# Kernel optimization log

Measured on AMD Instinct MI355X. Metric: run time of the kernel, lower is better.

The kernel has to match this reference:

```python
import jax, jax.numpy as jnp
import numpy as np

H = 2048  # hidden_dim == input_dim


def _lstm_step(x, h, c, Wih, Whh, bih, bhh):
    # x: [1, in], h/c: [1, H]; PyTorch gate order: i, f, g, o along 4H axis
    gates = x @ Wih.T + h @ Whh.T + bih + bhh  # [1, 4H]
    i, f, g, o = jnp.split(gates, 4, axis=-1)
    c2 = jax.nn.sigmoid(f) * c + jax.nn.sigmoid(i) * jnp.tanh(g)
    h2 = jax.nn.sigmoid(o) * jnp.tanh(c2)
    return h2, c2


def setup_inputs() -> dict:
    key = jax.random.key(0)
    ks = jax.random.split(key, 20)
    s = 0.02
    inp = {
        "x": jax.random.normal(ks[0], (1,), dtype=jnp.float32),
        "input_hidden": jax.random.normal(ks[1], (3, 1, H), dtype=jnp.float32),
        "input_cell": jax.random.normal(ks[2], (3, 1, H), dtype=jnp.float32),
        # layer 0: input_size = 1
        "Wih0": jax.random.normal(ks[3], (4 * H, 1), dtype=jnp.float32) * s,
        "Whh0": jax.random.normal(ks[4], (4 * H, H), dtype=jnp.float32) * s,
        "bih0": jax.random.normal(ks[5], (4 * H,), dtype=jnp.float32) * s,
        "bhh0": jax.random.normal(ks[6], (4 * H,), dtype=jnp.float32) * s,
        # layers 1, 2: input_size = H
        "Wih1": jax.random.normal(ks[7], (4 * H, H), dtype=jnp.float32) * s,
        "Whh1": jax.random.normal(ks[8], (4 * H, H), dtype=jnp.float32) * s,
        "bih1": jax.random.normal(ks[9], (4 * H,), dtype=jnp.float32) * s,
        "bhh1": jax.random.normal(ks[10], (4 * H,), dtype=jnp.float32) * s,
        "Wih2": jax.random.normal(ks[11], (4 * H, H), dtype=jnp.float32) * s,
        "Whh2": jax.random.normal(ks[12], (4 * H, H), dtype=jnp.float32) * s,
        "bih2": jax.random.normal(ks[13], (4 * H,), dtype=jnp.float32) * s,
        "bhh2": jax.random.normal(ks[14], (4 * H,), dtype=jnp.float32) * s,
        # output projection: Linear(H, 1)
        "Wout": jax.random.normal(ks[15], (1, H), dtype=jnp.float32) * s,
        "bout": jax.random.normal(ks[16], (1,), dtype=jnp.float32) * s,
    }
    return inp


def reference(x, input_hidden, input_cell,
              Wih0, Whh0, bih0, bhh0,
              Wih1, Whh1, bih1, bhh1,
              Wih2, Whh2, bih2, bhh2,
              Wout, bout):
    # x.reshape((1,1,1)) in torch -> single timestep, batch 1, feature 1
    inp = x.reshape(1, 1)  # [batch=1, in=1]
    params = [(Wih0, Whh0, bih0, bhh0),
              (Wih1, Whh1, bih1, bhh1),
              (Wih2, Whh2, bih2, bhh2)]
    hs, cs = [], []
    layer_in = inp
    for l, (Wih, Whh, bih, bhh) in enumerate(params):  # fixed 3 layers
        h2, c2 = _lstm_step(layer_in, input_hidden[l], input_cell[l], Wih, Whh, bih, bhh)
        hs.append(h2)
        cs.append(c2)
        layer_in = h2
    hidden_n = jnp.stack(hs, axis=0)  # [3, 1, H]
    cell_n = jnp.stack(cs, axis=0)    # [3, 1, H]
    # top-layer output [1,1,H] -> Linear -> [1,1,1]
    y = (layer_in @ Wout.T + bout).reshape(1, 1, 1)
    return y, hidden_n, cell_n
```

## Files before the change

### kernel.cpp

```cpp
#include <hip/hip_runtime.h>
#include <math.h>

#define H 2048

__device__ __forceinline__ float sigmoidf_(float v) {
    return 1.0f / (1.0f + expf(-v));
}

__device__ __forceinline__ float dot4(float4 a, float4 b) {
    return a.x * b.x + a.y * b.y + a.z * b.z + a.w * b.w;
}

__device__ __forceinline__ void bfly4(float& a, float& b, float& c, float& d) {
#pragma unroll
    for (int off = 32; off > 0; off >>= 1) {
        a += __shfl_down(a, off, 64);
        b += __shfl_down(b, off, 64);
        c += __shfl_down(c, off, 64);
        d += __shfl_down(d, off, 64);
    }
}

__global__ __launch_bounds__(256, 4)
void lstm_layer(const float* __restrict__ Wih, const float* __restrict__ Whh,
                const float* __restrict__ bih, const float* __restrict__ bhh,
                const float* __restrict__ xin,
                const float* __restrict__ hin,
                const float* __restrict__ cin,
                float* __restrict__ hout, float* __restrict__ cout)
{
    const int t    = blockIdx.x;
    const int tid  = threadIdx.x;
    const int w    = tid >> 6;
    const int lane = tid & 63;
    const int idx  = (w << 7) + lane;

    const float b_i = bih[t]         + bhh[t];
    const float b_f = bih[H + t]     + bhh[H + t];
    const float b_g = bih[2 * H + t] + bhh[2 * H + t];
    const float b_o = bih[3 * H + t] + bhh[3 * H + t];
    const float cprev = cin[t];

    const float4* x4  = (const float4*)xin;
    const float4* h4  = (const float4*)hin;
    const float4* wi0 = (const float4*)(Wih + (size_t)t * H);
    const float4* wh0 = (const float4*)(Whh + (size_t)t * H);
    const float4* wi1 = (const float4*)(Wih + (size_t)(H + t) * H);
    const float4* wh1 = (const float4*)(Whh + (size_t)(H + t) * H);
    const float4* wi2 = (const float4*)(Wih + (size_t)(2 * H + t) * H);
    const float4* wh2 = (const float4*)(Whh + (size_t)(2 * H + t) * H);
    const float4* wi3 = (const float4*)(Wih + (size_t)(3 * H + t) * H);
    const float4* wh3 = (const float4*)(Whh + (size_t)(3 * H + t) * H);

    const float4 xv0 = x4[idx], xv1 = x4[idx + 64];
    const float4 hv0 = h4[idx], hv1 = h4[idx + 64];
    float4 Ai0 = wi0[idx], Ai1 = wi0[idx + 64];
    float4 Ah0 = wh0[idx], Ah1 = wh0[idx + 64];
    float4 Bi0 = wi1[idx], Bi1 = wi1[idx + 64];
    float4 Bh0 = wh1[idx], Bh1 = wh1[idx + 64];
    float4 Ci0 = wi2[idx], Ci1 = wi2[idx + 64];
    float4 Ch0 = wh2[idx], Ch1 = wh2[idx + 64];
    float4 Di0 = wi3[idx], Di1 = wi3[idx + 64];
    float4 Dh0 = wh3[idx], Dh1 = wh3[idx + 64];
    __builtin_amdgcn_sched_barrier(0);

    float s_i = (dot4(Ai0, xv0) + dot4(Ah0, hv0)) + (dot4(Ai1, xv1) + dot4(Ah1, hv1));
    float s_f = (dot4(Bi0, xv0) + dot4(Bh0, hv0)) + (dot4(Bi1, xv1) + dot4(Bh1, hv1));
    float s_g = (dot4(Ci0, xv0) + dot4(Ch0, hv0)) + (dot4(Ci1, xv1) + dot4(Ch1, hv1));
    float s_o = (dot4(Di0, xv0) + dot4(Dh0, hv0)) + (dot4(Di1, xv1) + dot4(Dh1, hv1));

    bfly4(s_i, s_f, s_g, s_o);

    __shared__ float part[4][4];
    if (lane == 0) {
        part[w][0] = s_i; part[w][1] = s_f; part[w][2] = s_g; part[w][3] = s_o;
    }
    __syncthreads();
    if (tid == 0) {
        float gi = part[0][0] + part[1][0] + part[2][0] + part[3][0] + b_i;
        float gf = part[0][1] + part[1][1] + part[2][1] + part[3][1] + b_f;
        float gg = part[0][2] + part[1][2] + part[2][2] + part[3][2] + b_g;
        float go = part[0][3] + part[1][3] + part[2][3] + part[3][3] + b_o;
        float c2 = sigmoidf_(gf) * cprev + sigmoidf_(gi) * tanhf(gg);
        float h2 = sigmoidf_(go) * tanhf(c2);
        cout[t] = c2;
        hout[t] = h2;
    }
}

__global__ __launch_bounds__(256, 4)
void lstm_layer0(const float* __restrict__ Wih0,
                 const float* __restrict__ Whh,
                 const float* __restrict__ bih, const float* __restrict__ bhh,
                 const float* __restrict__ xs,
                 const float* __restrict__ hin, const float* __restrict__ cin,
                 float* __restrict__ hout, float* __restrict__ cout)
{
    const int t    = blockIdx.x;
    const int tid  = threadIdx.x;
    const int w    = tid >> 6;
    const int lane = tid & 63;
    const int idx  = (w << 7) + lane;

    const float x = xs[0];
    const float b_i = bih[t]         + bhh[t]         + x * Wih0[t];
    const float b_f = bih[H + t]     + bhh[H + t]     + x * Wih0[H + t];
    const float b_g = bih[2 * H + t] + bhh[2 * H + t] + x * Wih0[2 * H + t];
    const float b_o = bih[3 * H + t] + bhh[3 * H + t] + x * Wih0[3 * H + t];
    const float cprev = cin[t];

    const float4* h4 = (const float4*)hin;
    const float4* wi = (const float4*)(Whh + (size_t)t * H);
    const float4* wf = (const float4*)(Whh + (size_t)(H + t) * H);
    const float4* wg = (const float4*)(Whh + (size_t)(2 * H + t) * H);
    const float4* wo = (const float4*)(Whh + (size_t)(3 * H + t) * H);

    const float4 hv0 = h4[idx], hv1 = h4[idx + 64];
    float4 a0 = wi[idx], a1 = wi[idx + 64];
    float4 b0 = wf[idx], b1 = wf[idx + 64];
    float4 c0 = wg[idx], c1 = wg[idx + 64];
    float4 d0 = wo[idx], d1 = wo[idx + 64];
    __builtin_amdgcn_sched_barrier(0);

    float s_i = dot4(a0, hv0) + dot4(a1, hv1);
    float s_f = dot4(b0, hv0) + dot4(b1, hv1);
    float s_g = dot4(c0, hv0) + dot4(c1, hv1);
    float s_o = dot4(d0, hv0) + dot4(d1, hv1);

    bfly4(s_i, s_f, s_g, s_o);

    __shared__ float part[4][4];
    if (lane == 0) {
        part[w][0] = s_i; part[w][1] = s_f; part[w][2] = s_g; part[w][3] = s_o;
    }
    __syncthreads();
    if (tid == 0) {
        float gi = part[0][0] + part[1][0] + part[2][0] + part[3][0] + b_i;
        float gf = part[0][1] + part[1][1] + part[2][1] + part[3][1] + b_f;
        float gg = part[0][2] + part[1][2] + part[2][2] + part[3][2] + b_g;
        float go = part[0][3] + part[1][3] + part[2][3] + part[3][3] + b_o;
        float c2 = sigmoidf_(gf) * cprev + sigmoidf_(gi) * tanhf(gg);
        float h2 = sigmoidf_(go) * tanhf(c2);
        cout[t] = c2;
        hout[t] = h2;
    }
}

__global__ __launch_bounds__(256)
void out_proj(const float* __restrict__ Wout,
              const float* __restrict__ bout,
              const float* __restrict__ h,
              float* __restrict__ y)
{
    __shared__ float partl[4];
    const int tid = threadIdx.x;
    const float4* W4 = (const float4*)Wout;
    const float4* h4 = (const float4*)h;
    float acc = 0.0f;
#pragma unroll
    for (int k = 0; k < 2; ++k) {
        int i = tid + 256 * k;
        float4 a = W4[i];
        float4 b = h4[i];
        acc += a.x * b.x + a.y * b.y + a.z * b.z + a.w * b.w;
    }
#pragma unroll
    for (int off = 32; off > 0; off >>= 1) acc += __shfl_down(acc, off, 64);
    if ((tid & 63) == 0) partl[tid >> 6] = acc;
    __syncthreads();
    if (tid == 0) y[0] = partl[0] + partl[1] + partl[2] + partl[3] + bout[0];
}

extern "C" void kernel_launch(void* const* d_in, const int* in_sizes, int n_in,
                              void* d_out, int out_size, void* d_ws, size_t ws_size,
                              hipStream_t stream) {
    const float* x    = (const float*)d_in[0];
    const float* hin  = (const float*)d_in[1];
    const float* cin  = (const float*)d_in[2];
    const float* Wih0 = (const float*)d_in[3];
    const float* Whh0 = (const float*)d_in[4];
    const float* bih0 = (const float*)d_in[5];
    const float* bhh0 = (const float*)d_in[6];
    const float* Wih1 = (const float*)d_in[7];
    const float* Whh1 = (const float*)d_in[8];
    const float* bih1 = (const float*)d_in[9];
    const float* bhh1 = (const float*)d_in[10];
    const float* Wih2 = (const float*)d_in[11];
    const float* Whh2 = (const float*)d_in[12];
    const float* bih2 = (const float*)d_in[13];
    const float* bhh2 = (const float*)d_in[14];
    const float* Wout = (const float*)d_in[15];
    const float* bout = (const float*)d_in[16];

    float* out = (float*)d_out;
    float* y  = out;
    float* hN = out + 1;
    float* cN = out + 1 + 3 * H;

    lstm_layer0<<<2048, 256, 0, stream>>>(Wih0, Whh0, bih0, bhh0, x,
                                          hin, cin, hN, cN);
    lstm_layer<<<2048, 256, 0, stream>>>(Wih1, Whh1, bih1, bhh1,
                                         hN, hin + H, cin + H,
                                         hN + H, cN + H);
    lstm_layer<<<2048, 256, 0, stream>>>(Wih2, Whh2, bih2, bhh2,
                                         hN + H, hin + 2 * H, cin + 2 * H,
                                         hN + 2 * H, cN + 2 * H);
    out_proj<<<1, 256, 0, stream>>>(Wout, bout, hN + 2 * H, y);
}
```

Before: 326.2 us.

## Stage LSTM weight rows into LDS via async global_load_lds, one gate per wave

Each block now copies its gate weight rows straight from global memory into LDS with the direct global-to-LDS load builtin, instead of loading them into registers. After that, each wave computes one full gate dot product rather than a quarter of all four gates, which removes the four-way butterfly and the cross-wave partial sums. The layers need 32 KB and 64 KB of dynamic LDS per block, which limits occupancy to about two blocks per CU for the main layers. It also adds a barrier and LDS read traffic on what was a purely bandwidth-bound weight stream.

```diff
diff --git a/kernel.cpp b/kernel.cpp
--- a/kernel.cpp
+++ b/kernel.cpp
@@ -11,17 +11,15 @@
     return a.x * b.x + a.y * b.y + a.z * b.z + a.w * b.w;
 }
 
-__device__ __forceinline__ void bfly4(float& a, float& b, float& c, float& d) {
-#pragma unroll
-    for (int off = 32; off > 0; off >>= 1) {
-        a += __shfl_down(a, off, 64);
-        b += __shfl_down(b, off, 64);
-        c += __shfl_down(c, off, 64);
-        d += __shfl_down(d, off, 64);
-    }
+__device__ __forceinline__ void stage16(const float* g, float* l) {
+    __builtin_amdgcn_global_load_lds(
+        (const __attribute__((address_space(1))) void*)g,
+        (__attribute__((address_space(3))) void*)l, 16, 0, 0);
 }
 
-__global__ __launch_bounds__(256, 4)
+extern __shared__ float lds[];
+
+__global__ __launch_bounds__(256)
 void lstm_layer(const float* __restrict__ Wih, const float* __restrict__ Whh,
                 const float* __restrict__ bih, const float* __restrict__ bhh,
                 const float* __restrict__ xin,
@@ -33,62 +31,49 @@
     const int tid  = threadIdx.x;
     const int w    = tid >> 6;
     const int lane = tid & 63;
-    const int idx  = (w << 7) + lane;
 
-    const float b_i = bih[t]         + bhh[t];
-    const float b_f = bih[H + t]     + bhh[H + t];
-    const float b_g = bih[2 * H + t] + bhh[2 * H + t];
-    const float b_o = bih[3 * H + t] + bhh[3 * H + t];
-    const float cprev = cin[t];
+#pragma unroll
+    for (int j = 0; j < 16; ++j) {
+        const int u = (j << 2) | w;
+        const int r = u >> 3, q = u & 7;
+        const float* row = (r < 4) ? (Wih + (size_t)(r * H + t) * H)
+                                   : (Whh + (size_t)((r - 4) * H + t) * H);
+        stage16(row + q * 256 + lane * 4, lds + u * 256);
+    }
 
-    const float4* x4  = (const float4*)xin;
-    const float4* h4  = (const float4*)hin;
-    const float4* wi0 = (const float4*)(Wih + (size_t)t * H);
-    const float4* wh0 = (const float4*)(Whh + (size_t)t * H);
-    const float4* wi1 = (const float4*)(Wih + (size_t)(H + t) * H);
-    const float4* wh1 = (const float4*)(Whh + (size_t)(H + t) * H);
-    const float4* wi2 = (const float4*)(Wih + (size_t)(2 * H + t) * H);
-    const float4* wh2 = (const float4*)(Whh + (size_t)(2 * H + t) * H);
-    const float4* wi3 = (const float4*)(Wih + (size_t)(3 * H + t) * H);
-    const float4* wh3 = (const float4*)(Whh + (size_t)(3 * H + t) * H);
+    const float bias = bih[w * H + t] + bhh[w * H + t];
 
-    const float4 xv0 = x4[idx], xv1 = x4[idx + 64];
-    const float4 hv0 = h4[idx], hv1 = h4[idx + 64];
-    float4 Ai0 = wi0[idx], Ai1 = wi0[idx + 64];
-    float4 Ah0 = wh0[idx], Ah1 = wh0[idx + 64];
-    float4 Bi0 = wi1[idx], Bi1 = wi1[idx + 64];
-    float4 Bh0 = wh1[idx], Bh1 = wh1[idx + 64];
-    float4 Ci0 = wi2[idx], Ci1 = wi2[idx + 64];
-    float4 Ch0 = wh2[idx], Ch1 = wh2[idx + 64];
-    float4 Di0 = wi3[idx], Di1 = wi3[idx + 64];
-    float4 Dh0 = wh3[idx], Dh1 = wh3[idx + 64];
-    __builtin_amdgcn_sched_barrier(0);
+    __syncthreads();
 
-    float s_i = (dot4(Ai0, xv0) + dot4(Ah0, hv0)) + (dot4(Ai1, xv1) + dot4(Ah1, hv1));
-    float s_f = (dot4(Bi0, xv0) + dot4(Bh0, hv0)) + (dot4(Bi1, xv1) + dot4(Bh1, hv1));
-    float s_g = (dot4(Ci0, xv0) + dot4(Ch0, hv0)) + (dot4(Ci1, xv1) + dot4(Ch1, hv1));
-    float s_o = (dot4(Di0, xv0) + dot4(Dh0, hv0)) + (dot4(Di1, xv1) + dot4(Dh1, hv1));
+    const float4* wiq = (const float4*)lds + (size_t)w * 512;
+    const float4* whq = (const float4*)lds + (size_t)(4 + w) * 512;
+    const float4* xq  = (const float4*)xin;
+    const float4* hq  = (const float4*)hin;
+    float a0 = 0.0f, a1 = 0.0f;
+#pragma unroll
+    for (int j = 0; j < 8; ++j) {
+        const int i = lane + 64 * j;
+        a0 += dot4(wiq[i], xq[i]);
+        a1 += dot4(whq[i], hq[i]);
+    }
+    float s = a0 + a1;
+#pragma unroll
+    for (int off = 32; off > 0; off >>= 1) s += __shfl_down(s, off, 64);
 
-    bfly4(s_i, s_f, s_g, s_o);
-
-    __shared__ float part[4][4];
-    if (lane == 0) {
-        part[w][0] = s_i; part[w][1] = s_f; part[w][2] = s_g; part[w][3] = s_o;
-    }
+    __shared__ float gates[4];
+    if (lane == 0) gates[w] = s + bias;
     __syncthreads();
     if (tid == 0) {
-        float gi = part[0][0] + part[1][0] + part[2][0] + part[3][0] + b_i;
-        float gf = part[0][1] + part[1][1] + part[2][1] + part[3][1] + b_f;
-        float gg = part[0][2] + part[1][2] + part[2][2] + part[3][2] + b_g;
-        float go = part[0][3] + part[1][3] + part[2][3] + part[3][3] + b_o;
-        float c2 = sigmoidf_(gf) * cprev + sigmoidf_(gi) * tanhf(gg);
-        float h2 = sigmoidf_(go) * tanhf(c2);
+        const float gi = gates[0], gf = gates[1], gg = gates[2], go = gates[3];
+        const float cprev = cin[t];
+        const float c2 = sigmoidf_(gf) * cprev + sigmoidf_(gi) * tanhf(gg);
+        const float h2 = sigmoidf_(go) * tanhf(c2);
         cout[t] = c2;
         hout[t] = h2;
     }
 }
 
-__global__ __launch_bounds__(256, 4)
+__global__ __launch_bounds__(256)
 void lstm_layer0(const float* __restrict__ Wih0,
                  const float* __restrict__ Whh,
                  const float* __restrict__ bih, const float* __restrict__ bhh,
@@ -100,47 +85,40 @@
     const int tid  = threadIdx.x;
     const int w    = tid >> 6;
     const int lane = tid & 63;
-    const int idx  = (w << 7) + lane;
 
-    const float x = xs[0];
-    const float b_i = bih[t]         + bhh[t]         + x * Wih0[t];
-    const float b_f = bih[H + t]     + bhh[H + t]     + x * Wih0[H + t];
-    const float b_g = bih[2 * H + t] + bhh[2 * H + t] + x * Wih0[2 * H + t];
-    const float b_o = bih[3 * H + t] + bhh[3 * H + t] + x * Wih0[3 * H + t];
-    const float cprev = cin[t];
+#pragma unroll
+    for (int j = 0; j < 8; ++j) {
+        const int u = (j << 2) | w;
+        const int r = u >> 3, q = u & 7;
+        stage16(Whh + (size_t)(r * H + t) * H + q * 256 + lane * 4,
+                lds + u * 256);
+    }
 
-    const float4* h4 = (const float4*)hin;
-    const float4* wi = (const float4*)(Whh + (size_t)t * H);
-    const float4* wf = (const float4*)(Whh + (size_t)(H + t) * H);
-    const float4* wg = (const float4*)(Whh + (size_t)(2 * H + t) * H);
-    const float4* wo = (const float4*)(Whh + (size_t)(3 * H + t) * H);
+    const float bias = bih[w * H + t] + bhh[w * H + t] + xs[0] * Wih0[w * H + t];
 
-    const float4 hv0 = h4[idx], hv1 = h4[idx + 64];
-    float4 a0 = wi[idx], a1 = wi[idx + 64];
-    float4 b0 = wf[idx], b1 = wf[idx + 64];
-    float4 c0 = wg[idx], c1 = wg[idx + 64];
-    float4 d0 = wo[idx], d1 = wo[idx + 64];
-    __builtin_amdgcn_sched_barrier(0);
+    __syncthreads();
 
-    float s_i = dot4(a0, hv0) + dot4(a1, hv1);
-    float s_f = dot4(b0, hv0) + dot4(b1, hv1);
-    float s_g = dot4(c0, hv0) + dot4(c1, hv1);
-    float s_o = dot4(d0, hv0) + dot4(d1, hv1);
+    const float4* wq_ = (const float4*)lds + (size_t)w * 512;
+    const float4* hq  = (const float4*)hin;
+    float a0 = 0.0f, a1 = 0.0f;
+#pragma unroll
+    for (int j = 0; j < 8; j += 2) {
+        const int i0 = lane + 64 * j, i1 = lane + 64 * (j + 1);
+        a0 += dot4(wq_[i0], hq[i0]);
+        a1 += dot4(wq_[i1], hq[i1]);
+    }
+    float s = a0 + a1;
+#pragma unroll
+    for (int off = 32; off > 0; off >>= 1) s += __shfl_down(s, off, 64);
 
-    bfly4(s_i, s_f, s_g, s_o);
-
-    __shared__ float part[4][4];
-    if (lane == 0) {
-        part[w][0] = s_i; part[w][1] = s_f; part[w][2] = s_g; part[w][3] = s_o;
-    }
+    __shared__ float gates[4];
+    if (lane == 0) gates[w] = s + bias;
     __syncthreads();
     if (tid == 0) {
-        float gi = part[0][0] + part[1][0] + part[2][0] + part[3][0] + b_i;
-        float gf = part[0][1] + part[1][1] + part[2][1] + part[3][1] + b_f;
-        float gg = part[0][2] + part[1][2] + part[2][2] + part[3][2] + b_g;
-        float go = part[0][3] + part[1][3] + part[2][3] + part[3][3] + b_o;
-        float c2 = sigmoidf_(gf) * cprev + sigmoidf_(gi) * tanhf(gg);
-        float h2 = sigmoidf_(go) * tanhf(c2);
+        const float gi = gates[0], gf = gates[1], gg = gates[2], go = gates[3];
+        const float cprev = cin[t];
+        const float c2 = sigmoidf_(gf) * cprev + sigmoidf_(gi) * tanhf(gg);
+        const float h2 = sigmoidf_(go) * tanhf(c2);
         cout[t] = c2;
         hout[t] = h2;
     }
@@ -197,13 +175,13 @@
     float* hN = out + 1;
     float* cN = out + 1 + 3 * H;
 
-    lstm_layer0<<<2048, 256, 0, stream>>>(Wih0, Whh0, bih0, bhh0, x,
-                                          hin, cin, hN, cN);
-    lstm_layer<<<2048, 256, 0, stream>>>(Wih1, Whh1, bih1, bhh1,
-                                         hN, hin + H, cin + H,
-                                         hN + H, cN + H);
-    lstm_layer<<<2048, 256, 0, stream>>>(Wih2, Whh2, bih2, bhh2,
-                                         hN + H, hin + 2 * H, cin + 2 * H,
-                                         hN + 2 * H, cN + 2 * H);
+    lstm_layer0<<<2048, 256, 32768, stream>>>(Wih0, Whh0, bih0, bhh0, x,
+                                              hin, cin, hN, cN);
+    lstm_layer<<<2048, 256, 65536, stream>>>(Wih1, Whh1, bih1, bhh1,
+                                             hN, hin + H, cin + H,
+                                             hN + H, cN + H);
+    lstm_layer<<<2048, 256, 65536, stream>>>(Wih2, Whh2, bih2, bhh2,
+                                             hN + H, hin + 2 * H, cin + 2 * H,
+                                             hN + 2 * H, cN + 2 * H);
     out_proj<<<1, 256, 0, stream>>>(Wout, bout, hN + 2 * H, y);
 }
```

Result: no change. 331.0 us (+1.5%).
